# Kernel optimization log

Hardware: AMD Instinct MI355X
Metric: run time of the kernel (lower is better)

Reference implementation:

```python
import jax, jax.numpy as jnp
import numpy as np

B, S, D = 4, 1024, 2048
NH, NKV, HD = 16, 8, 128
N_EXP, TOP_K, RANK, ALPHA = 4, 2, 16, 32
LORA_SCALE = ALPHA / RANK
EPS = 1e-6
NEG_INF = -1e9


def setup_inputs() -> dict:
    key = jax.random.key(0)
    ks = jax.random.split(key, 12)
    inv_freq = 1.0 / (10000.0 ** (jnp.arange(0, HD, 2, dtype=jnp.float32) / HD))
    pos = jnp.arange(S, dtype=jnp.float32)
    freqs = pos[:, None] * inv_freq[None, :]            # [S, HD/2]
    emb = jnp.concatenate([freqs, freqs], axis=-1)      # [S, HD]
    cos = jnp.broadcast_to(jnp.cos(emb)[None], (B, S, HD))
    sin = jnp.broadcast_to(jnp.sin(emb)[None], (B, S, HD))
    s = 0.02
    return {
        "hidden_states": jax.random.normal(ks[0], (B, S, D), jnp.float32),
        "cos": cos,
        "sin": sin,
        "Wq": jax.random.normal(ks[1], (NH * HD, D), jnp.float32) * s,
        "Wk": jax.random.normal(ks[2], (NKV * HD, D), jnp.float32) * s,
        "Wv": jax.random.normal(ks[3], (NKV * HD, D), jnp.float32) * s,
        "Wo": jax.random.normal(ks[4], (D, NH * HD), jnp.float32) * s,
        "q_norm_w": jnp.ones((HD,), jnp.float32),
        "k_norm_w": jnp.ones((HD,), jnp.float32),
        "gate_w": jax.random.normal(ks[5], (N_EXP, D), jnp.float32) * s,
        "loraA": jax.random.normal(ks[6], (N_EXP, RANK, NH * HD), jnp.float32) * s,
        "loraB": jax.random.normal(ks[7], (N_EXP, D, RANK), jnp.float32) * s,
    }


def _rms_norm(x, w):
    # per-head-dim RMSNorm (Qwen3 style), computed in fp32
    var = jnp.mean(jnp.square(x.astype(jnp.float32)), axis=-1, keepdims=True)
    return (x.astype(jnp.float32) * jax.lax.rsqrt(var + EPS)).astype(x.dtype) * w


def _rotate_half(x):
    x1, x2 = jnp.split(x, 2, axis=-1)
    return jnp.concatenate([-x2, x1], axis=-1)


def reference(hidden_states, cos, sin, Wq, Wk, Wv, Wo, q_norm_w, k_norm_w, gate_w, loraA, loraB):
    b, s, d = hidden_states.shape
    scaling = HD ** -0.5

    # ---- router (top-k of softmax over 4 experts) ----
    flat = hidden_states.reshape(-1, d)                       # [T, D]
    router_logits = flat @ gate_w.T                           # [T, E]
    probs = jax.nn.softmax(router_logits.astype(jnp.float32), axis=-1)
    top_w, top_idx = jax.lax.top_k(probs, TOP_K)              # [T, K]
    top_w = top_w.astype(hidden_states.dtype)
    # dense per-expert weight: [T, E]
    expert_w = jnp.sum(jax.nn.one_hot(top_idx, N_EXP, dtype=top_w.dtype) * top_w[..., None], axis=1)

    # ---- QKV projections + per-head RMSNorm ----
    q = (hidden_states @ Wq.T).reshape(b, s, NH, HD)
    k = (hidden_states @ Wk.T).reshape(b, s, NKV, HD)
    v = (hidden_states @ Wv.T).reshape(b, s, NKV, HD)
    q = _rms_norm(q, q_norm_w).transpose(0, 2, 1, 3)          # [B, NH, S, HD]
    k = _rms_norm(k, k_norm_w).transpose(0, 2, 1, 3)          # [B, NKV, S, HD]
    v = v.transpose(0, 2, 1, 3)

    # ---- RoPE ----
    c, sn = cos[:, None], sin[:, None]                        # [B, 1, S, HD]
    q = q * c + _rotate_half(q) * sn
    k = k * c + _rotate_half(k) * sn

    # ---- GQA repeat + eager attention ----
    n_rep = NH // NKV
    k = jnp.repeat(k, n_rep, axis=1)
    v = jnp.repeat(v, n_rep, axis=1)
    attn = jnp.einsum('bhqd,bhkd->bhqk', q, k) * scaling
    causal = jnp.tril(jnp.ones((s, s), bool))
    attn = jnp.where(causal[None, None], attn, NEG_INF)
    attn_w = jax.nn.softmax(attn.astype(jnp.float32), axis=-1).astype(q.dtype)
    attn_out = jnp.einsum('bhqk,bhkd->bqhd', attn_w, v).reshape(b, s, NH * HD)

    # ---- base output projection + LoRA expert mixture ----
    base = attn_out @ Wo.T                                    # [B, S, D]
    x = attn_out.reshape(-1, NH * HD)                         # [T, NH*HD]
    h = jnp.einsum('td,erd->ter', x, loraA)                   # [T, E, R]
    delta = jnp.einsum('ter,edr->ted', h, loraB) * LORA_SCALE # [T, E, D]
    expert_out = jnp.einsum('te,ted->td', expert_w, delta).reshape(b, s, d)

    return base + expert_out
```

## Files before the change

### kernel.cpp

```cpp
#include <hip/hip_runtime.h>
#include <hip/hip_bf16.h>

#define S_LEN   1024
#define BATCH   4
#define DMODEL  2048
#define NHEADS  16
#define NKVH    8
#define HEADD   128
#define NTOK    4096
#define QKV_CH  4096

typedef __bf16 bf16x8 __attribute__((ext_vector_type(8)));
typedef float  f32x4  __attribute__((ext_vector_type(4)));

__device__ __forceinline__ float bf2f(unsigned short u) {
    return __uint_as_float(((unsigned)u) << 16);
}
__device__ __forceinline__ ushort f2bu(float f) {
    union { __hip_bfloat16 h; ushort u; } c;
    c.h = __float2bfloat16(f);
    return c.u;
}
__device__ __forceinline__ void gl_lds16(const ushort* g, ushort* l) {
    __builtin_amdgcn_global_load_lds(
        (const __attribute__((address_space(1))) void*)g,
        (__attribute__((address_space(3))) void*)l,
        16, 0, 0);
}

__global__ __launch_bounds__(256) void wcast_kernel(const float* __restrict__ Wq,
                                                    const float* __restrict__ Wk,
                                                    const float* __restrict__ Wv,
                                                    const float* __restrict__ Wo,
                                                    const float* __restrict__ lA,
                                                    __hip_bfloat16* __restrict__ wqkv,
                                                    __hip_bfloat16* __restrict__ wo,
                                                    __hip_bfloat16* __restrict__ acat) {
    int i = blockIdx.x * 256 + threadIdx.x;
    const float* src; __hip_bfloat16* dst; int off;
    if (i < 1048576)      { src = Wq; dst = wqkv;           off = i; }
    else if (i < 1572864) { src = Wk; dst = wqkv + 4194304; off = i - 1048576; }
    else if (i < 2097152) { src = Wv; dst = wqkv + 6291456; off = i - 1572864; }
    else if (i < 3145728) { src = Wo; dst = wo;             off = i - 2097152; }
    else if (i < 3178496) { src = lA; dst = acat;           off = i - 3145728; }
    else return;
    float4 v = ((const float4*)src)[off];
    union { ushort4 u; __hip_bfloat16 h[4]; } r;
    r.h[0] = __float2bfloat16(v.x);
    r.h[1] = __float2bfloat16(v.y);
    r.h[2] = __float2bfloat16(v.z);
    r.h[3] = __float2bfloat16(v.w);
    ((ushort4*)dst)[off] = r.u;
}

__global__ __launch_bounds__(256) void btrans_kernel(const float* __restrict__ lB,
                                                     ushort* __restrict__ Bt) {
    int idx = blockIdx.x * 256 + threadIdx.x;
    int d = idx >> 6, er = idx & 63;
    int e = er >> 4, r = er & 15;
    Bt[idx] = f2bu(lB[((size_t)e * DMODEL + d) * 16 + r]);
}

__global__ __launch_bounds__(256) void gatecast_kernel(const float* __restrict__ X,
                                                       const float* __restrict__ GW,
                                                       __hip_bfloat16* __restrict__ Xb,
                                                       float* __restrict__ EW) {
    __shared__ float red[4][257];
    const int t = blockIdx.x, tid = threadIdx.x;
    const float* x = X + (size_t)t * DMODEL;
    __hip_bfloat16* xb = Xb + (size_t)t * DMODEL;
    float p0 = 0.f, p1 = 0.f, p2 = 0.f, p3 = 0.f;
#pragma unroll
    for (int c = 0; c < 2; c++) {
        int i4 = tid + c * 256;
        float4 v = ((const float4*)x)[i4];
        union { ushort4 u; __hip_bfloat16 h[4]; } r;
        r.h[0] = __float2bfloat16(v.x);
        r.h[1] = __float2bfloat16(v.y);
        r.h[2] = __float2bfloat16(v.z);
        r.h[3] = __float2bfloat16(v.w);
        ((ushort4*)xb)[i4] = r.u;
        int d = i4 * 4;
        const float* g0 = GW + d;
        p0 += v.x * g0[0] + v.y * g0[1] + v.z * g0[2] + v.w * g0[3];
        const float* g1 = GW + DMODEL + d;
        p1 += v.x * g1[0] + v.y * g1[1] + v.z * g1[2] + v.w * g1[3];
        const float* g2 = GW + 2 * DMODEL + d;
        p2 += v.x * g2[0] + v.y * g2[1] + v.z * g2[2] + v.w * g2[3];
        const float* g3 = GW + 3 * DMODEL + d;
        p3 += v.x * g3[0] + v.y * g3[1] + v.z * g3[2] + v.w * g3[3];
    }
    red[0][tid] = p0; red[1][tid] = p1; red[2][tid] = p2; red[3][tid] = p3;
    __syncthreads();
    for (int s = 128; s > 0; s >>= 1) {
        if (tid < s) {
            red[0][tid] += red[0][tid + s];
            red[1][tid] += red[1][tid + s];
            red[2][tid] += red[2][tid + s];
            red[3][tid] += red[3][tid + s];
        }
        __syncthreads();
    }
    if (tid == 0) {
        float l[4] = { red[0][0], red[1][0], red[2][0], red[3][0] };
        float mx = fmaxf(fmaxf(l[0], l[1]), fmaxf(l[2], l[3]));
        float pe[4], sum = 0.f;
        for (int e = 0; e < 4; e++) { pe[e] = __expf(l[e] - mx); sum += pe[e]; }
        float inv = 1.0f / sum;
        for (int e = 0; e < 4; e++) pe[e] *= inv;
        int i1 = 0;
        for (int e = 1; e < 4; e++) if (pe[e] > pe[i1]) i1 = e;
        int i2 = -1;
        for (int e = 0; e < 4; e++) if (e != i1 && (i2 < 0 || pe[e] > pe[i2])) i2 = e;
        float o[4] = {0.f, 0.f, 0.f, 0.f};
        o[i1] = pe[i1]; o[i2] = pe[i2];
        float* ew = EW + (size_t)t * 4;
        ew[0] = o[0]; ew[1] = o[1]; ew[2] = o[2]; ew[3] = o[3];
    }
}

#define LDSA0 0
#define LDSB0 16384
#define LDSA1 32768
#define LDSB1 49152

#define FENCE_BAR() do { asm volatile("" ::: "memory"); __builtin_amdgcn_s_barrier(); } while (0)

__device__ __forceinline__ void stage_half(const ushort* src, ushort* dst, int ld) {
    gl_lds16(src, dst);
    gl_lds16(src + (size_t)64 * ld, dst + 4096);
}

#define PHASE_MFMA_PRE()  do { \
    asm volatile("" ::: "memory"); \
    __builtin_amdgcn_s_barrier(); \
    asm volatile("s_waitcnt lgkmcnt(0)" ::: "memory"); \
    __builtin_amdgcn_sched_barrier(0); \
    __builtin_amdgcn_s_setprio(1); } while (0)

#define PHASE_MFMA_POST() do { \
    __builtin_amdgcn_s_setprio(0); } while (0)

__device__ __forceinline__ void ktile(const ushort* As, const ushort* Bs,
                                      f32x4 (&acc)[8][4],
                                      int aBase, int bBase, int cs0, int cs1,
                                      const ushort* s1s, ushort* s1d, bool s12en,
                                      const ushort* s2s, ushort* s2d,
                                      const ushort* s3s, ushort* s3d, bool s34en,
                                      const ushort* s4s, ushort* s4d,
                                      int K, bool lastVm)
{
    bf16x8 a0[4][2], a1[4][2], b0[2][2], b1[2][2];

#pragma unroll
    for (int ii = 0; ii < 4; ii++) {
        a0[ii][0] = *(const bf16x8*)(As + aBase + ii * 2048 + cs0);
        a0[ii][1] = *(const bf16x8*)(As + aBase + ii * 2048 + cs1);
    }
#pragma unroll
    for (int jj = 0; jj < 2; jj++) {
        b0[jj][0] = *(const bf16x8*)(Bs + bBase + jj * 4096 + cs0);
        b0[jj][1] = *(const bf16x8*)(Bs + bBase + jj * 4096 + cs1);
    }
    if (s12en) stage_half(s1s, s1d, K);
    PHASE_MFMA_PRE();
#pragma unroll
    for (int k = 0; k < 2; k++)
#pragma unroll
        for (int ii = 0; ii < 4; ii++)
#pragma unroll
            for (int jj = 0; jj < 2; jj++)
                acc[ii][2 * jj] = __builtin_amdgcn_mfma_f32_16x16x32_bf16(
                    a0[ii][k], b0[jj][k], acc[ii][2 * jj], 0, 0, 0);
    PHASE_MFMA_POST();
    FENCE_BAR();

#pragma unroll
    for (int jj = 0; jj < 2; jj++) {
        b1[jj][0] = *(const bf16x8*)(Bs + bBase + 8192 + jj * 4096 + cs0);
        b1[jj][1] = *(const bf16x8*)(Bs + bBase + 8192 + jj * 4096 + cs1);
    }
    if (s12en) stage_half(s2s, s2d, K);
    PHASE_MFMA_PRE();
#pragma unroll
    for (int k = 0; k < 2; k++)
#pragma unroll
        for (int ii = 0; ii < 4; ii++)
#pragma unroll
            for (int jj = 0; jj < 2; jj++)
                acc[ii][1 + 2 * jj] = __builtin_amdgcn_mfma_f32_16x16x32_bf16(
                    a0[ii][k], b1[jj][k], acc[ii][1 + 2 * jj], 0, 0, 0);
    PHASE_MFMA_POST();
    FENCE_BAR();

#pragma unroll
    for (int ii = 0; ii < 4; ii++) {
        a1[ii][0] = *(const bf16x8*)(As + aBase + 8192 + ii * 2048 + cs0);
        a1[ii][1] = *(const bf16x8*)(As + aBase + 8192 + ii * 2048 + cs1);
    }
    if (s34en) stage_half(s3s, s3d, K);
    PHASE_MFMA_PRE();
#pragma unroll
    for (int k = 0; k < 2; k++)
#pragma unroll
        for (int ii = 0; ii < 4; ii++)
#pragma unroll
            for (int jj = 0; jj < 2; jj++)
                acc[4 + ii][2 * jj] = __builtin_amdgcn_mfma_f32_16x16x32_bf16(
                    a1[ii][k], b0[jj][k], acc[4 + ii][2 * jj], 0, 0, 0);
    PHASE_MFMA_POST();
    FENCE_BAR();

    if (s34en) stage_half(s4s, s4d, K);
    asm volatile("" ::: "memory");
    __builtin_amdgcn_s_barrier();
    __builtin_amdgcn_sched_barrier(0);
    __builtin_amdgcn_s_setprio(1);
#pragma unroll
    for (int k = 0; k < 2; k++)
#pragma unroll
        for (int ii = 0; ii < 4; ii++)
#pragma unroll
            for (int jj = 0; jj < 2; jj++)
                acc[4 + ii][1 + 2 * jj] = __builtin_amdgcn_mfma_f32_16x16x32_bf16(
                    a1[ii][k], b1[jj][k], acc[4 + ii][1 + 2 * jj], 0, 0, 0);
    __builtin_amdgcn_s_setprio(0);
    if (lastVm) { asm volatile("s_waitcnt vmcnt(0)" ::: "memory"); }
    else        { asm volatile("s_waitcnt vmcnt(4)" ::: "memory"); }
    __builtin_amdgcn_s_barrier();
}

__global__ __launch_bounds__(512, 2) void gemm256(const ushort* __restrict__ A,
                                                  const ushort* __restrict__ B,
                                                  float* __restrict__ C,
                                                  int M, int N, int K) {
    __shared__ __align__(16) ushort lds[65536];
    const int tid  = threadIdx.x;
    const int wave = tid >> 6, lane = tid & 63;
    const int l16  = lane & 15, quad = lane >> 4;
    const int wm = wave >> 2, wn = wave & 3;

    const int wg0 = blockIdx.x;
    const int swz = (wg0 & 7) * 32 + (wg0 >> 3);
    const int m0 = (swz >> 4) * 256, n0 = (swz & 15) * 256;

    const int srow = tid >> 3;
    const int scol = ((tid & 7) * 8) ^ ((srow & 7) << 3);
    const ushort* aSrc = A + (size_t)(m0 + srow) * K + scol;
    const ushort* bSrc = B + (size_t)(n0 + srow) * K + scol;

    const int aBase = (wm * 16 + l16) * 64;
    const int bBase = (wn * 16 + l16) * 64;
    const int cs0 = ((0 + quad) ^ (l16 & 7)) * 8;
    const int cs1 = ((4 + quad) ^ (l16 & 7)) * 8;

    f32x4 acc[8][4];
#pragma unroll
    for (int i = 0; i < 8; i++)
#pragma unroll
        for (int j = 0; j < 4; j++) acc[i][j] = (f32x4){0.f, 0.f, 0.f, 0.f};

    const int NT = K >> 6;

    const ushort* A0s = lds + LDSA0;
    const ushort* B0s = lds + LDSB0;
    const ushort* A1s = lds + LDSA1;
    const ushort* B1s = lds + LDSB1;

    stage_half(aSrc,                     lds + LDSA0 + tid * 8, K);
    stage_half(aSrc + (size_t)128 * K,   lds + LDSA0 + 8192 + tid * 8, K);
    stage_half(bSrc,                     lds + LDSB0 + tid * 8, K);
    stage_half(bSrc + (size_t)128 * K,   lds + LDSB0 + 8192 + tid * 8, K);
    stage_half(aSrc + 64,                lds + LDSA1 + tid * 8, K);
    stage_half(bSrc + 64,                lds + LDSB1 + tid * 8, K);
    asm volatile("s_waitcnt vmcnt(4)" ::: "memory");
    __builtin_amdgcn_s_barrier();

    for (int t = 0; t + 1 < NT; t += 2) {
        const bool s34 = (t + 2) < NT, s78 = (t + 3) < NT;
        const int k1 = (t + 1) * 64, k2 = (t + 2) * 64, k3 = (t + 3) * 64;

        ktile(A0s, B0s, acc, aBase, bBase, cs0, cs1,
              aSrc + (size_t)128 * K + k1, lds + LDSA1 + 8192 + tid * 8, true,
              bSrc + (size_t)128 * K + k1, lds + LDSB1 + 8192 + tid * 8,
              aSrc + k2,                   lds + LDSA0 + tid * 8, s34,
              bSrc + k2,                   lds + LDSB0 + tid * 8,
              K, !s34);

        ktile(A1s, B1s, acc, aBase, bBase, cs0, cs1,
              aSrc + (size_t)128 * K + k2, lds + LDSA0 + 8192 + tid * 8, s34,
              bSrc + (size_t)128 * K + k2, lds + LDSB0 + 8192 + tid * 8,
              aSrc + k3,                   lds + LDSA1 + tid * 8, s78,
              bSrc + k3,                   lds + LDSB1 + tid * 8,
              K, !s78);
    }

    float* crow = C + (size_t)(m0 + wm * 16 + quad * 4) * N + n0 + wn * 16 + l16;
#pragma unroll
    for (int i = 0; i < 8; i++) {
        float* cpi = crow + (size_t)((i & 3) * 32 + (i >> 2) * 128) * N;
#pragma unroll
        for (int r = 0; r < 4; r++)
#pragma unroll
            for (int j = 0; j < 4; j++)
                cpi[(size_t)r * N + ((j & 1) * 128 + (j >> 1) * 64)] = acc[i][j][r];
    }
}

__global__ __launch_bounds__(256) void gemm_bt_lora(const ushort* __restrict__ A,
                                                    const ushort* __restrict__ B,
                                                    const ushort* __restrict__ A2,
                                                    const ushort* __restrict__ B2,
                                                    float* __restrict__ C) {
    __shared__ ushort As[128 * 32];
    __shared__ ushort Bs[128 * 32];
    const int tid  = threadIdx.x;
    const int wave = tid >> 6, lane = tid & 63;
    const int l16  = lane & 15, quad = lane >> 4;
    const int m0 = blockIdx.y * 128, n0 = blockIdx.x * 128;
    const int wm = (wave >> 1) * 64, wn = (wave & 1) * 64;
    const int K = DMODEL, N = DMODEL;

    f32x4 acc[4][4];
#pragma unroll
    for (int i = 0; i < 4; i++)
#pragma unroll
        for (int j = 0; j < 4; j++) acc[i][j] = (f32x4){0.f, 0.f, 0.f, 0.f};

    const int r1 = tid >> 2, kg1 = (tid & 3) * 8;
    const int r2 = (tid + 256) >> 2, kg2 = ((tid + 256) & 3) * 8;

    for (int k0 = 0; k0 < K; k0 += 32) {
        __syncthreads();
        gl_lds16(A + (size_t)(m0 + r1) * K + k0 + kg1, As + tid * 8);
        gl_lds16(B + (size_t)(n0 + r1) * K + k0 + kg1, Bs + tid * 8);
        gl_lds16(A + (size_t)(m0 + r2) * K + k0 + kg2, As + (tid + 256) * 8);
        gl_lds16(B + (size_t)(n0 + r2) * K + k0 + kg2, Bs + (tid + 256) * 8);
        __syncthreads();
        bf16x8 af[4], bfr[4];
#pragma unroll
        for (int i = 0; i < 4; i++) {
            af[i]  = *(const bf16x8*)(As + (wm + i * 16 + l16) * 32 + quad * 8);
            bfr[i] = *(const bf16x8*)(Bs + (wn + i * 16 + l16) * 32 + quad * 8);
        }
#pragma unroll
        for (int i = 0; i < 4; i++)
#pragma unroll
            for (int j = 0; j < 4; j++)
                acc[i][j] = __builtin_amdgcn_mfma_f32_16x16x32_bf16(af[i], bfr[j], acc[i][j], 0, 0, 0);
    }

#pragma unroll
    for (int k0 = 0; k0 < 64; k0 += 32) {
        __syncthreads();
        gl_lds16(A2 + (size_t)(m0 + r1) * 64 + k0 + kg1, As + tid * 8);
        gl_lds16(B2 + (size_t)(n0 + r1) * 64 + k0 + kg1, Bs + tid * 8);
        gl_lds16(A2 + (size_t)(m0 + r2) * 64 + k0 + kg2, As + (tid + 256) * 8);
        gl_lds16(B2 + (size_t)(n0 + r2) * 64 + k0 + kg2, Bs + (tid + 256) * 8);
        __syncthreads();
        bf16x8 af[4], bfr[4];
#pragma unroll
        for (int i = 0; i < 4; i++) {
            af[i]  = *(const bf16x8*)(As + (wm + i * 16 + l16) * 32 + quad * 8);
            bfr[i] = *(const bf16x8*)(Bs + (wn + i * 16 + l16) * 32 + quad * 8);
        }
#pragma unroll
        for (int i = 0; i < 4; i++)
#pragma unroll
            for (int j = 0; j < 4; j++)
                acc[i][j] = __builtin_amdgcn_mfma_f32_16x16x32_bf16(af[i], bfr[j], acc[i][j], 0, 0, 0);
    }

#pragma unroll
    for (int i = 0; i < 4; i++)
#pragma unroll
        for (int j = 0; j < 4; j++)
#pragma unroll
            for (int r = 0; r < 4; r++) {
                int m = m0 + wm + i * 16 + quad * 4 + r;
                int n = n0 + wn + j * 16 + l16;
                C[(size_t)m * N + n] = acc[i][j][r];
            }
}

__global__ __launch_bounds__(256) void lora_h_kernel(const ushort* __restrict__ X,
                                                     const ushort* __restrict__ Acat,
                                                     const float* __restrict__ EW,
                                                     ushort* __restrict__ G) {
    __shared__ ushort As[64 * 32];
    __shared__ ushort Bs[64 * 32];
    const int tid = threadIdx.x;
    const int wave = tid >> 6, lane = tid & 63;
    const int l16 = lane & 15, quad = lane >> 4;
    const int m0 = blockIdx.x * 64;

    f32x4 acc[4];
#pragma unroll
    for (int nt = 0; nt < 4; nt++) acc[nt] = (f32x4){0.f, 0.f, 0.f, 0.f};

    const int r1 = tid >> 2, kg1 = (tid & 3) * 8;

    for (int k0 = 0; k0 < DMODEL; k0 += 32) {
        __syncthreads();
        gl_lds16(X + (size_t)(m0 + r1) * DMODEL + k0 + kg1, As + tid * 8);
        gl_lds16(Acat + (size_t)r1 * DMODEL + k0 + kg1, Bs + tid * 8);
        __syncthreads();
        bf16x8 af = *(const bf16x8*)(As + (wave * 16 + l16) * 32 + quad * 8);
#pragma unroll
        for (int nt = 0; nt < 4; nt++) {
            bf16x8 bfr = *(const bf16x8*)(Bs + (nt * 16 + l16) * 32 + quad * 8);
            acc[nt] = __builtin_amdgcn_mfma_f32_16x16x32_bf16(af, bfr, acc[nt], 0, 0, 0);
        }
    }
#pragma unroll
    for (int nt = 0; nt < 4; nt++)
#pragma unroll
        for (int r = 0; r < 4; r++) {
            int m = m0 + wave * 16 + quad * 4 + r;
            float wsc = 2.0f * EW[(size_t)m * 4 + nt];
            G[(size_t)m * 64 + nt * 16 + l16] = f2bu(acc[nt][r] * wsc);
        }
}

__global__ __launch_bounds__(256) void normrope_kernel(const float* __restrict__ QKV,
                                                       const float* __restrict__ cosb,
                                                       const float* __restrict__ sinb,
                                                       const float* __restrict__ qw,
                                                       const float* __restrict__ kw,
                                                       ushort* __restrict__ Qb,
                                                       ushort* __restrict__ Kb) {
    const int wave = threadIdx.x >> 6, lane = threadIdx.x & 63;
    const int r = blockIdx.x * 4 + wave;
    const float* p; const float* w; int t; ushort* dst; float scale;
    if (r < NTOK * NHEADS) {
        t = r >> 4;
        int h = r & 15;
        p = QKV + (size_t)t * QKV_CH + h * HEADD;
        w = qw; scale = 0.08838834764831845f;
        int b = t >> 10, s = t & 1023;
        dst = Qb + ((size_t)((b * 16 + h) * 1024 + s)) * HEADD;
    } else {
        int r2 = r - NTOK * NHEADS;
        t = r2 >> 3;
        int kv = r2 & 7;
        p = QKV + (size_t)t * QKV_CH + 2048 + kv * HEADD;
        w = kw; scale = 1.0f;
        int b = t >> 10, s = t & 1023;
        dst = Kb + ((size_t)((b * 8 + kv) * 1024 + s)) * HEADD;
    }
    float xl = p[lane], xh = p[lane + 64];
    float ss = xl * xl + xh * xh;
#pragma unroll
    for (int mask = 1; mask < 64; mask <<= 1) ss += __shfl_xor(ss, mask);
    float rstd = rsqrtf(ss * (1.0f / 128.0f) + 1e-6f);
    float nl = xl * rstd * w[lane];
    float nh = xh * rstd * w[lane + 64];
    const float* cp = cosb + (size_t)t * HEADD;
    const float* sp = sinb + (size_t)t * HEADD;
    float ol = nl * cp[lane]      - nh * sp[lane];
    float oh = nh * cp[lane + 64] + nl * sp[lane + 64];
    dst[lane]      = f2bu(ol * scale);
    dst[lane + 64] = f2bu(oh * scale);
}

__global__ __launch_bounds__(256) void vtrans_kernel(const float* __restrict__ QKV,
                                                     ushort* __restrict__ Vt) {
    __shared__ float Ts[64][129];
    const int blk = blockIdx.x;
    const int sc = blk & 15;
    const int kvb = blk >> 4;
    const int s0 = sc * 64;
    const float* src = QKV + ((size_t)((kvb >> 3) * 1024 + s0)) * QKV_CH + 3072 + (kvb & 7) * HEADD;
    for (int c = threadIdx.x; c < 2048; c += 256) {
        int s = c >> 5, d0 = (c & 31) * 4;
        float4 v = *(const float4*)(src + (size_t)s * QKV_CH + d0);
        Ts[s][d0] = v.x; Ts[s][d0 + 1] = v.y; Ts[s][d0 + 2] = v.z; Ts[s][d0 + 3] = v.w;
    }
    __syncthreads();
    ushort* dst = Vt + ((size_t)kvb * HEADD) * S_LEN + s0;
    for (int c = threadIdx.x; c < 1024; c += 256) {
        int d = c >> 3, s8 = (c & 7) * 8;
        union { ushort u[8]; uint4 v; } pk;
#pragma unroll
        for (int j = 0; j < 8; j++) pk.u[j] = f2bu(Ts[s8 + j][d]);
        *(uint4*)(dst + (size_t)d * S_LEN + s8) = pk.v;
    }
}

#define KPITCH 136
#define VPITCH 72
__global__ __launch_bounds__(256) void fattn_kernel(const ushort* __restrict__ Qb,
                                                    const ushort* __restrict__ Kb,
                                                    const ushort* __restrict__ Vt,
                                                    __hip_bfloat16* __restrict__ O) {
    __shared__ __align__(16) ushort Ks[64 * KPITCH];
    __shared__ __align__(16) ushort Vs[128 * VPITCH];
    __shared__ __align__(16) ushort Ps[4 * 16 * VPITCH];
    const int tid = threadIdx.x;
    const int wq = tid >> 6, lane = tid & 63;
    const int l16 = lane & 15, quad = lane >> 4;
    const int qblk = 15 - (blockIdx.x >> 6);
    const int bh = blockIdx.x & 63;
    const int b = bh >> 4, h = bh & 15;
    const int kvb = b * 8 + (h >> 1);
    const int q0 = qblk * 64;
    const int qbase = q0 + wq * 16;

    bf16x8 qf[4];
    const ushort* qrow = Qb + ((size_t)bh * S_LEN + qbase + l16) * HEADD;
#pragma unroll
    for (int kt = 0; kt < 4; kt++)
        qf[kt] = *(const bf16x8*)(qrow + kt * 32 + quad * 8);

    f32x4 oacc[8];
#pragma unroll
    for (int dt = 0; dt < 8; dt++) oacc[dt] = (f32x4){0.f, 0.f, 0.f, 0.f};
    float l[4] = { 0.f, 0.f, 0.f, 0.f };

    const ushort* kbase = Kb + (size_t)kvb * S_LEN * HEADD;
    const ushort* vbase = Vt + (size_t)kvb * HEADD * S_LEN;
    const int ntiles = qblk + 1;

    for (int kb = 0; kb < ntiles; kb++) {
        const int k0 = kb * 64;
        __syncthreads();
        for (int c = tid; c < 1024; c += 256) {
            int row = c >> 4, col = (c & 15) * 8;
            *(uint4*)(Ks + row * KPITCH + col) =
                *(const uint4*)(kbase + (size_t)(k0 + row) * HEADD + col);
        }
        for (int c = tid; c < 1024; c += 256) {
            int row = c >> 3, col = (c & 7) * 8;
            *(uint4*)(Vs + row * VPITCH + col) =
                *(const uint4*)(vbase + (size_t)row * S_LEN + k0 + col);
        }
        __syncthreads();

        f32x4 sacc[4];
#pragma unroll
        for (int nt = 0; nt < 4; nt++) sacc[nt] = (f32x4){0.f, 0.f, 0.f, 0.f};
#pragma unroll
        for (int kt = 0; kt < 4; kt++) {
#pragma unroll
            for (int nt = 0; nt < 4; nt++) {
                bf16x8 kf = *(const bf16x8*)(Ks + (nt * 16 + l16) * KPITCH + kt * 32 + quad * 8);
                sacc[nt] = __builtin_amdgcn_mfma_f32_16x16x32_bf16(qf[kt], kf, sacc[nt], 0, 0, 0);
            }
        }

#pragma unroll
        for (int r = 0; r < 4; r++) {
            const int qg = qbase + quad * 4 + r;
#pragma unroll
            for (int nt = 0; nt < 4; nt++) {
                int kg = k0 + nt * 16 + l16;
                float p = (kg <= qg) ? __expf(sacc[nt][r]) : 0.f;
                l[r] += p;
                Ps[wq * 16 * VPITCH + (quad * 4 + r) * VPITCH + nt * 16 + l16] = f2bu(p);
            }
        }

#pragma unroll
        for (int kt2 = 0; kt2 < 2; kt2++) {
            bf16x8 pf = *(const bf16x8*)(Ps + wq * 16 * VPITCH + l16 * VPITCH + kt2 * 32 + quad * 8);
#pragma unroll
            for (int dt = 0; dt < 8; dt++) {
                bf16x8 vf = *(const bf16x8*)(Vs + (dt * 16 + l16) * VPITCH + kt2 * 32 + quad * 8);
                oacc[dt] = __builtin_amdgcn_mfma_f32_16x16x32_bf16(pf, vf, oacc[dt], 0, 0, 0);
            }
        }
    }

#pragma unroll
    for (int r = 0; r < 4; r++) {
        float lr = l[r];
        lr += __shfl_xor(lr, 1);
        lr += __shfl_xor(lr, 2);
        lr += __shfl_xor(lr, 4);
        lr += __shfl_xor(lr, 8);
        float inv = 1.0f / lr;
        size_t base = ((size_t)(b * S_LEN + qbase + quad * 4 + r)) * (NHEADS * HEADD) + h * HEADD;
#pragma unroll
        for (int dt = 0; dt < 8; dt++)
            O[base + dt * 16 + l16] = __float2bfloat16(oacc[dt][r] * inv);
    }
}

extern "C" void kernel_launch(void* const* d_in, const int* in_sizes, int n_in,
                              void* d_out, int out_size, void* d_ws, size_t ws_size,
                              hipStream_t stream) {
    const float* hidden = (const float*)d_in[0];
    const float* cosb   = (const float*)d_in[1];
    const float* sinb   = (const float*)d_in[2];
    const float* Wq     = (const float*)d_in[3];
    const float* Wk     = (const float*)d_in[4];
    const float* Wv     = (const float*)d_in[5];
    const float* Wo     = (const float*)d_in[6];
    const float* qnw    = (const float*)d_in[7];
    const float* knw    = (const float*)d_in[8];
    const float* gw     = (const float*)d_in[9];
    const float* lA     = (const float*)d_in[10];
    const float* lB     = (const float*)d_in[11];
    float* out = (float*)d_out;

    char* ws = (char*)d_ws;
    __hip_bfloat16* hid_bf  = (__hip_bfloat16*)ws;
    __hip_bfloat16* wqkv_bf = (__hip_bfloat16*)(ws + (16u << 20));
    __hip_bfloat16* wo_bf   = (__hip_bfloat16*)(ws + (32u << 20));
    float*          qkv     = (float*)(ws + (40u << 20));
    __hip_bfloat16* attn_bf = (__hip_bfloat16*)(ws + (40u << 20));
    ushort*         Qb      = (ushort*)ws;
    ushort*         Kb      = (ushort*)(ws + (16u << 20));
    ushort*         Vt      = (ushort*)(ws + (24u << 20));
    ushort*         Acat    = (ushort*)(ws + (104u << 20));
    ushort*         Bt      = (ushort*)(ws + (104u << 20) + (256u << 10));
    ushort*         G       = (ushort*)(ws + (104u << 20) + (512u << 10));
    float*          ew      = (float*)(ws + (105u << 20));

    wcast_kernel<<<12416, 256, 0, stream>>>(Wq, Wk, Wv, Wo, lA,
                                            wqkv_bf, wo_bf, (__hip_bfloat16*)Acat);
    gatecast_kernel<<<4096, 256, 0, stream>>>(hidden, gw, hid_bf, ew);
    btrans_kernel<<<512, 256, 0, stream>>>(lB, Bt);

    gemm256<<<256, 512, 0, stream>>>((const ushort*)hid_bf, (const ushort*)wqkv_bf,
                                     qkv, NTOK, QKV_CH, DMODEL);

    normrope_kernel<<<24576, 256, 0, stream>>>(qkv, cosb, sinb, qnw, knw, Qb, Kb);
    vtrans_kernel<<<512, 256, 0, stream>>>(qkv, Vt);

    fattn_kernel<<<1024, 256, 0, stream>>>(Qb, Kb, Vt, attn_bf);

    lora_h_kernel<<<64, 256, 0, stream>>>((const ushort*)attn_bf, Acat, ew, G);

    gemm_bt_lora<<<dim3(16, 32), 256, 0, stream>>>((const ushort*)attn_bf, (const ushort*)wo_bf,
                                                   G, Bt, out);
}
```

Measured before the change: 379.4 us.

## Fuse QK RMSNorm, RoPE and V transpose into QKV GEMM epilogue

Moves the per-head RMSNorm, RoPE and Q scaling into the epilogue of the QKV projection GEMM, and writes V transposed to bf16 through LDS. This removes the fp32 QKV intermediate round trip to memory and two separate kernel launches. The epilogue reduces sums of squares across waves in LDS and needs extra barriers and scattered bf16 stores. It also adds an lgkmcnt wait in the k-tile loop and moves workspace buffers around.

```diff
diff --git a/kernel.cpp b/kernel.cpp
--- a/kernel.cpp
+++ b/kernel.cpp
@@ -163,6 +163,7 @@
         b0[jj][1] = *(const bf16x8*)(Bs + bBase + jj * 4096 + cs1);
     }
     if (s12en) stage_half(s1s, s1d, K);
+    asm volatile("s_waitcnt lgkmcnt(8)" ::: "memory");
     PHASE_MFMA_PRE();
 #pragma unroll
     for (int k = 0; k < 2; k++)
@@ -232,8 +233,14 @@
 
 __global__ __launch_bounds__(512, 2) void gemm256(const ushort* __restrict__ A,
                                                   const ushort* __restrict__ B,
-                                                  float* __restrict__ C,
-                                                  int M, int N, int K) {
+                                                  const float* __restrict__ cosb,
+                                                  const float* __restrict__ sinb,
+                                                  const float* __restrict__ qnw,
+                                                  const float* __restrict__ knw,
+                                                  ushort* __restrict__ Qb,
+                                                  ushort* __restrict__ Kb,
+                                                  ushort* __restrict__ Vt,
+                                                  int K) {
     __shared__ __align__(16) ushort lds[65536];
     const int tid  = threadIdx.x;
     const int wave = tid >> 6, lane = tid & 63;
@@ -295,15 +302,89 @@
               K, !s78);
     }
 
-    float* crow = C + (size_t)(m0 + wm * 16 + quad * 4) * N + n0 + wn * 16 + l16;
-#pragma unroll
-    for (int i = 0; i < 8; i++) {
-        float* cpi = crow + (size_t)((i & 3) * 32 + (i >> 2) * 128) * N;
-#pragma unroll
-        for (int r = 0; r < 4; r++)
-#pragma unroll
-            for (int j = 0; j < 4; j++)
-                cpi[(size_t)r * N + ((j & 1) * 128 + (j >> 1) * 64)] = acc[i][j][r];
+    const int nb = n0 >> 8;
+    if (nb < 12) {
+        const bool isQ = (nb < 8);
+        const float scale = isQ ? 0.08838834764831845f : 1.0f;
+        const float* nw = isQ ? qnw : knw;
+        const int d0 = wn * 16 + l16;
+        const float w0 = nw[d0], w1 = nw[d0 + 64];
+        float* fsq = (float*)lds;
+
+#pragma unroll
+        for (int i = 0; i < 8; i++)
+#pragma unroll
+            for (int r = 0; r < 4; r++) {
+                int rowl = (i & 3) * 32 + (i >> 2) * 128 + wm * 16 + quad * 4 + r;
+#pragma unroll
+                for (int h = 0; h < 2; h++) {
+                    float x1 = acc[i][h][r], x2 = acc[i][h + 2][r];
+                    float p = x1 * x1 + x2 * x2;
+                    p += __shfl_xor(p, 1);
+                    p += __shfl_xor(p, 2);
+                    p += __shfl_xor(p, 4);
+                    p += __shfl_xor(p, 8);
+                    if (l16 == 0) fsq[(rowl * 2 + h) * 4 + wn] = p;
+                }
+            }
+        __syncthreads();
+
+#pragma unroll
+        for (int i = 0; i < 8; i++)
+#pragma unroll
+            for (int r = 0; r < 4; r++) {
+                int rowl = (i & 3) * 32 + (i >> 2) * 128 + wm * 16 + quad * 4 + r;
+                int tok = m0 + rowl;
+                int b = tok >> 10, s = tok & 1023;
+                const float* cp = cosb + (size_t)tok * HEADD;
+                const float* sp = sinb + (size_t)tok * HEADD;
+                float cl = cp[d0], ch = cp[d0 + 64];
+                float sl = sp[d0], sh = sp[d0 + 64];
+#pragma unroll
+                for (int h = 0; h < 2; h++) {
+                    const float* q4 = fsq + (rowl * 2 + h) * 4;
+                    float ssq = q4[0] + q4[1] + q4[2] + q4[3];
+                    float rstd = rsqrtf(ssq * (1.0f / 128.0f) + 1e-6f);
+                    float n1 = acc[i][h][r] * rstd * w0;
+                    float n2 = acc[i][h + 2][r] * rstd * w1;
+                    float o1 = (n1 * cl - n2 * sl) * scale;
+                    float o2 = (n2 * ch + n1 * sh) * scale;
+                    ushort* dst;
+                    if (isQ) {
+                        int hq = (n0 >> 7) + h;
+                        dst = Qb + ((size_t)((b * 16 + hq) * 1024 + s)) * HEADD;
+                    } else {
+                        int kv = ((n0 - 2048) >> 7) + h;
+                        dst = Kb + ((size_t)((b * 8 + kv) * 1024 + s)) * HEADD;
+                    }
+                    dst[d0]      = f2bu(o1);
+                    dst[d0 + 64] = f2bu(o2);
+                }
+            }
+    } else {
+#pragma unroll
+        for (int i = 0; i < 8; i++)
+#pragma unroll
+            for (int j = 0; j < 4; j++) {
+                int coll = (j & 1) * 128 + (j >> 1) * 64 + wn * 16 + l16;
+                int xr = (coll & 7) << 3;
+#pragma unroll
+                for (int r = 0; r < 4; r++) {
+                    int rowl = (i & 3) * 32 + (i >> 2) * 128 + wm * 16 + quad * 4 + r;
+                    lds[coll * 256 + (rowl ^ xr)] = f2bu(acc[i][j][r]);
+                }
+            }
+        __syncthreads();
+        const int b = m0 >> 10, s0 = m0 & 1023;
+        const int kv0 = (n0 - 3072) >> 7;
+#pragma unroll
+        for (int g = 0; g < 16; g++) {
+            int gg = tid + g * 512;
+            int d = gg >> 5, sg = gg & 31;
+            uint4 v = *(const uint4*)(lds + d * 256 + ((sg * 8) ^ ((d & 7) << 3)));
+            int kv = kv0 + (d >> 7), dh = d & 127;
+            *(uint4*)(Vt + ((size_t)((b * 8 + kv) * 128 + dh)) * 1024 + s0 + sg * 8) = v;
+        }
     }
 }
 
@@ -420,71 +501,6 @@
             float wsc = 2.0f * EW[(size_t)m * 4 + nt];
             G[(size_t)m * 64 + nt * 16 + l16] = f2bu(acc[nt][r] * wsc);
         }
-}
-
-__global__ __launch_bounds__(256) void normrope_kernel(const float* __restrict__ QKV,
-                                                       const float* __restrict__ cosb,
-                                                       const float* __restrict__ sinb,
-                                                       const float* __restrict__ qw,
-                                                       const float* __restrict__ kw,
-                                                       ushort* __restrict__ Qb,
-                                                       ushort* __restrict__ Kb) {
-    const int wave = threadIdx.x >> 6, lane = threadIdx.x & 63;
-    const int r = blockIdx.x * 4 + wave;
-    const float* p; const float* w; int t; ushort* dst; float scale;
-    if (r < NTOK * NHEADS) {
-        t = r >> 4;
-        int h = r & 15;
-        p = QKV + (size_t)t * QKV_CH + h * HEADD;
-        w = qw; scale = 0.08838834764831845f;
-        int b = t >> 10, s = t & 1023;
-        dst = Qb + ((size_t)((b * 16 + h) * 1024 + s)) * HEADD;
-    } else {
-        int r2 = r - NTOK * NHEADS;
-        t = r2 >> 3;
-        int kv = r2 & 7;
-        p = QKV + (size_t)t * QKV_CH + 2048 + kv * HEADD;
-        w = kw; scale = 1.0f;
-        int b = t >> 10, s = t & 1023;
-        dst = Kb + ((size_t)((b * 8 + kv) * 1024 + s)) * HEADD;
-    }
-    float xl = p[lane], xh = p[lane + 64];
-    float ss = xl * xl + xh * xh;
-#pragma unroll
-    for (int mask = 1; mask < 64; mask <<= 1) ss += __shfl_xor(ss, mask);
-    float rstd = rsqrtf(ss * (1.0f / 128.0f) + 1e-6f);
-    float nl = xl * rstd * w[lane];
-    float nh = xh * rstd * w[lane + 64];
-    const float* cp = cosb + (size_t)t * HEADD;
-    const float* sp = sinb + (size_t)t * HEADD;
-    float ol = nl * cp[lane]      - nh * sp[lane];
-    float oh = nh * cp[lane + 64] + nl * sp[lane + 64];
-    dst[lane]      = f2bu(ol * scale);
-    dst[lane + 64] = f2bu(oh * scale);
-}
-
-__global__ __launch_bounds__(256) void vtrans_kernel(const float* __restrict__ QKV,
-                                                     ushort* __restrict__ Vt) {
-    __shared__ float Ts[64][129];
-    const int blk = blockIdx.x;
-    const int sc = blk & 15;
-    const int kvb = blk >> 4;
-    const int s0 = sc * 64;
-    const float* src = QKV + ((size_t)((kvb >> 3) * 1024 + s0)) * QKV_CH + 3072 + (kvb & 7) * HEADD;
-    for (int c = threadIdx.x; c < 2048; c += 256) {
-        int s = c >> 5, d0 = (c & 31) * 4;
-        float4 v = *(const float4*)(src + (size_t)s * QKV_CH + d0);
-        Ts[s][d0] = v.x; Ts[s][d0 + 1] = v.y; Ts[s][d0 + 2] = v.z; Ts[s][d0 + 3] = v.w;
-    }
-    __syncthreads();
-    ushort* dst = Vt + ((size_t)kvb * HEADD) * S_LEN + s0;
-    for (int c = threadIdx.x; c < 1024; c += 256) {
-        int d = c >> 3, s8 = (c & 7) * 8;
-        union { ushort u[8]; uint4 v; } pk;
-#pragma unroll
-        for (int j = 0; j < 8; j++) pk.u[j] = f2bu(Ts[s8 + j][d]);
-        *(uint4*)(dst + (size_t)d * S_LEN + s8) = pk.v;
-    }
 }
 
 #define KPITCH 136
@@ -607,11 +623,10 @@
     __hip_bfloat16* hid_bf  = (__hip_bfloat16*)ws;
     __hip_bfloat16* wqkv_bf = (__hip_bfloat16*)(ws + (16u << 20));
     __hip_bfloat16* wo_bf   = (__hip_bfloat16*)(ws + (32u << 20));
-    float*          qkv     = (float*)(ws + (40u << 20));
-    __hip_bfloat16* attn_bf = (__hip_bfloat16*)(ws + (40u << 20));
-    ushort*         Qb      = (ushort*)ws;
-    ushort*         Kb      = (ushort*)(ws + (16u << 20));
-    ushort*         Vt      = (ushort*)(ws + (24u << 20));
+    ushort*         Qb      = (ushort*)(ws + (40u << 20));
+    ushort*         Kb      = (ushort*)(ws + (56u << 20));
+    ushort*         Vt      = (ushort*)(ws + (64u << 20));
+    __hip_bfloat16* attn_bf = (__hip_bfloat16*)(ws + (72u << 20));
     ushort*         Acat    = (ushort*)(ws + (104u << 20));
     ushort*         Bt      = (ushort*)(ws + (104u << 20) + (256u << 10));
     ushort*         G       = (ushort*)(ws + (104u << 20) + (512u << 10));
@@ -623,10 +638,7 @@
     btrans_kernel<<<512, 256, 0, stream>>>(lB, Bt);
 
     gemm256<<<256, 512, 0, stream>>>((const ushort*)hid_bf, (const ushort*)wqkv_bf,
-                                     qkv, NTOK, QKV_CH, DMODEL);
-
-    normrope_kernel<<<24576, 256, 0, stream>>>(qkv, cosb, sinb, qnw, knw, Qb, Kb);
-    vtrans_kernel<<<512, 256, 0, stream>>>(qkv, Vt);
+                                     cosb, sinb, qnw, knw, Qb, Kb, Vt, DMODEL);
 
     fattn_kernel<<<1024, 256, 0, stream>>>(Qb, Kb, Vt, attn_bf);
 
```

Result: no change. 374.5 us (-1.3%).
